# Kernel tuning notes

Hardware: AMD Instinct MI355X
Metric: run time of the kernel (lower is better)

The kernel has to match this reference:

```python
import jax, jax.numpy as jnp
import numpy as np

D_MODEL = 1024
N_HEAD = 16
HEAD_DIM = D_MODEL // N_HEAD


def setup_inputs() -> dict:
    key = jax.random.key(0)
    ks = jax.random.split(key, 5)
    B, T = 2, 2048
    s = 1.0 / np.sqrt(D_MODEL)
    return {
        "x": jax.random.normal(ks[0], (B, T, D_MODEL), dtype=jnp.float32),
        "w_qkv": jax.random.normal(ks[1], (D_MODEL, 3 * D_MODEL), dtype=jnp.float32) * s,
        "b_qkv": jnp.zeros((3 * D_MODEL,), dtype=jnp.float32),
        "w_proj": jax.random.normal(ks[2], (D_MODEL, D_MODEL), dtype=jnp.float32) * s,
        "b_proj": jnp.zeros((D_MODEL,), dtype=jnp.float32),
    }


def reference(x, w_qkv, b_qkv, w_proj, b_proj):
    B, T, C = x.shape
    H, Dh = N_HEAD, HEAD_DIM
    scale = Dh ** -0.5
    qkv = x @ w_qkv + b_qkv                      # [B,T,3C]
    q, k, v = jnp.split(qkv, 3, axis=2)
    # [B,T,C] -> [B,H,T,Dh]
    q = q.reshape(B, T, H, Dh).transpose(0, 2, 1, 3)
    k = k.reshape(B, T, H, Dh).transpose(0, 2, 1, 3)
    v = v.reshape(B, T, H, Dh).transpose(0, 2, 1, 3)
    att = jnp.einsum("bhqd,bhkd->bhqk", q, k) * scale  # [B,H,T,T]
    causal = jnp.tril(jnp.ones((T, T), dtype=bool))
    att = jnp.where(causal, att, -jnp.inf)
    att = jax.nn.softmax(att, axis=-1)
    out = jnp.einsum("bhqk,bhkd->bhqd", att, v)  # [B,H,T,Dh]
    out = out.transpose(0, 2, 1, 3).reshape(B, T, C)
    return out @ w_proj + b_proj
```

## Files before the change

kernel.cpp:

```cpp
#include <hip/hip_runtime.h>
#include <hip/hip_bf16.h>

#define B_ 2
#define T_ 2048
#define C_ 1024
#define H_ 16
#define DH_ 64

typedef __attribute__((ext_vector_type(8))) short bf16x8;
typedef __attribute__((ext_vector_type(4))) float f32x4;
typedef __attribute__((ext_vector_type(4))) unsigned int u32x4;

#define DEVI static __device__ __forceinline__

DEVI unsigned short f2bf(float f) {
  unsigned int u = __float_as_uint(f);
  u = (u + 0x7fffu + ((u >> 16) & 1u)) >> 16;
  return (unsigned short)u;
}

DEVI f32x4 mfma16(bf16x8 a, bf16x8 b, f32x4 c) {
  return __builtin_amdgcn_mfma_f32_16x16x32_bf16(a, b, c, 0, 0, 0);
}

DEVI void gload_lds16(const unsigned short* g, unsigned short* l) {
  __builtin_amdgcn_global_load_lds(
      (const __attribute__((address_space(1))) unsigned int*)g,
      (__attribute__((address_space(3))) unsigned int*)l, 16, 0, 0);
}

DEVI unsigned int cvtpk_bf16(float lo, float hi) {
  unsigned int r;
  asm("v_cvt_pk_bf16_f32 %0, %1, %2" : "=v"(r) : "v"(lo), "v"(hi));
  return r;
}

DEVI int kperm(int kv) {
  return (kv & 3) | (((kv >> 3) & 1) << 2) | (((kv >> 5) & 1) << 3) |
         (((kv >> 2) & 1) << 4) | (((kv >> 4) & 1) << 5);
}

__global__ __launch_bounds__(256) void prep_kernel(
    const float* __restrict__ x, const float* __restrict__ w_qkv,
    const float* __restrict__ w_proj, unsigned short* __restrict__ xb,
    unsigned short* __restrict__ wqkvT, unsigned short* __restrict__ wprojT) {
  __shared__ float tile[32][33];
  int b = blockIdx.x, tid = threadIdx.x;
  if (b < 4096) {
    int i = b * 256 + tid;
    float4 v = reinterpret_cast<const float4*>(x)[i];
    ushort4 o;
    o.x = f2bf(v.x); o.y = f2bf(v.y); o.z = f2bf(v.z); o.w = f2bf(v.w);
    reinterpret_cast<ushort4*>(xb)[i] = o;
  } else {
    const float* in;
    unsigned short* out;
    int R, C, bb;
    if (b < 7168) { bb = b - 4096; in = w_qkv; out = wqkvT; R = 1024; C = 3072; }
    else          { bb = b - 7168; in = w_proj; out = wprojT; R = 1024; C = 1024; }
    int nbx = C >> 5;
    int c0 = (bb % nbx) * 32, r0 = (bb / nbx) * 32;
    int tx = tid & 31, ty = tid >> 5;
#pragma unroll
    for (int j = 0; j < 32; j += 8)
      tile[ty + j][tx] = in[(size_t)(r0 + ty + j) * C + c0 + tx];
    __syncthreads();
#pragma unroll
    for (int j = 0; j < 32; j += 8)
      out[(size_t)(c0 + ty + j) * R + r0 + tx] = f2bf(tile[tx][ty + j]);
  }
}

__global__ __launch_bounds__(256, 2) void gemm192_qkv(
    const unsigned short* __restrict__ A, const unsigned short* __restrict__ Bt,
    const float* __restrict__ bias,
    unsigned short* __restrict__ qbuf, unsigned short* __restrict__ kbuf,
    unsigned short* __restrict__ vtbuf) {
  __shared__ __attribute__((aligned(16))) unsigned short As[2][128 * 64];
  __shared__ __attribute__((aligned(16))) unsigned short Bs[2][192 * 64];
  const int Kd = 1024;
  int tid = threadIdx.x;
  int lane = tid & 63, w = tid >> 6;
  int wn = w;
  int lrow = lane & 15, lgrp = lane >> 4;

  int g = blockIdx.x;
  int gs = (g & 7) * 64 + (g >> 3);
  int by = gs >> 4, bx = gs & 15;
  int bm = by * 128, bn = bx * 192;
  const unsigned short* Ab = A + (size_t)bm * Kd;
  const unsigned short* Bb = Bt + (size_t)bn * Kd;

  int sL[2], scl[2];
#pragma unroll
  for (int it = 0; it < 2; ++it) {
    int c = tid + it * 256;
    int L = c >> 3, s = c & 7, v = s ^ (L & 7);
    sL[it] = L;
    scl[it] = (v >> 2) * 32 + (v & 3) * 8;
  }

  auto stgA = [&](int t, int h) {
    unsigned short* dst = As[t & 1] + h * 4096;
    int k0 = t << 6;
#pragma unroll
    for (int it = 0; it < 2; ++it)
      gload_lds16(Ab + (size_t)(h * 64 + sL[it]) * Kd + k0 + scl[it],
                  dst + (tid + it * 256) * 8);
  };
  auto stgB3 = [&](int t, int th) {
    unsigned short* dst = Bs[t & 1] + th * 4096;
    int k0 = t << 6;
#pragma unroll
    for (int it = 0; it < 2; ++it)
      gload_lds16(Bb + (size_t)(th * 64 + sL[it]) * Kd + k0 + scl[it],
                  dst + (tid + it * 256) * 8);
  };

  auto lda = [&](const unsigned short* buf, int mi, int kk) -> bf16x8 {
    int row = mi * 16 + lrow;
    int s = ((kk << 2) | lgrp) ^ (row & 7);
    return *reinterpret_cast<const bf16x8*>((const char*)buf + row * 128 + s * 16);
  };
  auto ldb = [&](const unsigned short* buf, int ni, int kk) -> bf16x8 {
    int row = wn * 48 + ni * 16 + lrow;
    int s = ((kk << 2) | lgrp) ^ (row & 7);
    return *reinterpret_cast<const bf16x8*>((const char*)buf + row * 128 + s * 16);
  };

  f32x4 acc[8][3] = {};
  bf16x8 bfr[3][2], af[2][2];

#define PHASE_TAIL                                          \
  __builtin_amdgcn_s_barrier();                             \
  asm volatile("s_waitcnt lgkmcnt(0)" ::: "memory");        \
  __builtin_amdgcn_sched_barrier(0);                        \
  __builtin_amdgcn_s_setprio(1);

#define MFMA_TRI(base)                                      \
  _Pragma("unroll") for (int ii = 0; ii < 2; ++ii)          \
  _Pragma("unroll") for (int ni = 0; ni < 3; ++ni) {        \
    acc[(base) + ii][ni] = mfma16(af[ii][0], bfr[ni][0], acc[(base) + ii][ni]); \
    acc[(base) + ii][ni] = mfma16(af[ii][1], bfr[ni][1], acc[(base) + ii][ni]); \
  }

#define PHASE_END                                           \
  __builtin_amdgcn_s_setprio(0);                            \
  __builtin_amdgcn_s_barrier();

  stgA(0, 0); stgA(0, 1);
  stgB3(0, 0); stgB3(0, 1); stgB3(0, 2);
  stgB3(1, 0); stgB3(1, 1); stgB3(1, 2);
  asm volatile("s_waitcnt vmcnt(6)" ::: "memory");
  __builtin_amdgcn_s_barrier();

#pragma unroll 1
  for (int j = 0; j < 8; ++j) {
    const bool nl = (j < 7);
    const int t1 = 2 * j + 1, t2 = 2 * j + 2, t3 = 2 * j + 3;

#pragma unroll
    for (int ni = 0; ni < 3; ++ni) { bfr[ni][0] = ldb(Bs[0], ni, 0); bfr[ni][1] = ldb(Bs[0], ni, 1); }
    af[0][0] = lda(As[0], 0, 0); af[0][1] = lda(As[0], 0, 1);
    af[1][0] = lda(As[0], 1, 0); af[1][1] = lda(As[0], 1, 1);
    stgA(t1, 0);
    PHASE_TAIL; MFMA_TRI(0); PHASE_END;

    af[0][0] = lda(As[0], 2, 0); af[0][1] = lda(As[0], 2, 1);
    af[1][0] = lda(As[0], 3, 0); af[1][1] = lda(As[0], 3, 1);
    stgA(t1, 1);
    if (nl) stgB3(t2, 0);
    PHASE_TAIL; MFMA_TRI(2); PHASE_END;

    af[0][0] = lda(As[0], 4, 0); af[0][1] = lda(As[0], 4, 1);
    af[1][0] = lda(As[0], 5, 0); af[1][1] = lda(As[0], 5, 1);
    if (nl) stgB3(t2, 1);
    PHASE_TAIL; MFMA_TRI(4); PHASE_END;

    af[0][0] = lda(As[0], 6, 0); af[0][1] = lda(As[0], 6, 1);
    af[1][0] = lda(As[0], 7, 0); af[1][1] = lda(As[0], 7, 1);
    if (nl) stgB3(t2, 2);
    PHASE_TAIL; MFMA_TRI(6);
    __builtin_amdgcn_s_setprio(0);
    if (nl) { asm volatile("s_waitcnt vmcnt(6)" ::: "memory"); }
    else    { asm volatile("s_waitcnt vmcnt(0)" ::: "memory"); }
    __builtin_amdgcn_s_barrier();

#pragma unroll
    for (int ni = 0; ni < 3; ++ni) { bfr[ni][0] = ldb(Bs[1], ni, 0); bfr[ni][1] = ldb(Bs[1], ni, 1); }
    af[0][0] = lda(As[1], 0, 0); af[0][1] = lda(As[1], 0, 1);
    af[1][0] = lda(As[1], 1, 0); af[1][1] = lda(As[1], 1, 1);
    if (nl) stgA(t2, 0);
    PHASE_TAIL; MFMA_TRI(0); PHASE_END;

    af[0][0] = lda(As[1], 2, 0); af[0][1] = lda(As[1], 2, 1);
    af[1][0] = lda(As[1], 3, 0); af[1][1] = lda(As[1], 3, 1);
    if (nl) { stgA(t2, 1); stgB3(t3, 0); }
    PHASE_TAIL; MFMA_TRI(2); PHASE_END;

    af[0][0] = lda(As[1], 4, 0); af[0][1] = lda(As[1], 4, 1);
    af[1][0] = lda(As[1], 5, 0); af[1][1] = lda(As[1], 5, 1);
    if (nl) stgB3(t3, 1);
    PHASE_TAIL; MFMA_TRI(4); PHASE_END;

    af[0][0] = lda(As[1], 6, 0); af[0][1] = lda(As[1], 6, 1);
    af[1][0] = lda(As[1], 7, 0); af[1][1] = lda(As[1], 7, 1);
    if (nl) stgB3(t3, 2);
    PHASE_TAIL; MFMA_TRI(6);
    __builtin_amdgcn_s_setprio(0);
    if (nl) { asm volatile("s_waitcnt vmcnt(6)" ::: "memory"); }
    __builtin_amdgcn_s_barrier();
  }
#undef PHASE_TAIL
#undef MFMA_TRI
#undef PHASE_END

  int c0 = bn + wn * 48;
#pragma unroll
  for (int ni = 0; ni < 3; ++ni) {
    int col = c0 + ni * 16 + lrow;
    float bv = bias[col];
    int which = col >> 10, cc = col & 1023;
    int h = cc >> 6, d = cc & 63;
#pragma unroll
    for (int mi = 0; mi < 8; ++mi) {
      int rowb = bm + mi * 16 + lgrp * 4;
      int b = rowb >> 11, tt = rowb & 2047;
      if (which == 2) {
        ushort4 pk;
        pk.x = f2bf(acc[mi][ni][0] + bv);
        pk.y = f2bf(acc[mi][ni][1] + bv);
        pk.z = f2bf(acc[mi][ni][2] + bv);
        pk.w = f2bf(acc[mi][ni][3] + bv);
        *reinterpret_cast<ushort4*>(vtbuf + ((size_t)((b * 16 + h) * 64 + d)) * T_ + tt) = pk;
      } else {
        unsigned short* dst = (which == 0) ? qbuf : kbuf;
        size_t base = ((size_t)(b * 16 + h) * T_ + tt) * DH_ + d;
#pragma unroll
        for (int r = 0; r < 4; ++r)
          dst[base + (size_t)r * DH_] = f2bf(acc[mi][ni][r] + bv);
      }
    }
  }
}

__global__ __launch_bounds__(256, 2) void gemm_proj(
    const unsigned short* __restrict__ A, const unsigned short* __restrict__ Bt,
    const float* __restrict__ bias, float* __restrict__ outp) {
  __shared__ __attribute__((aligned(16))) unsigned short As[2][128 * 64];
  __shared__ __attribute__((aligned(16))) unsigned short Bs[2][128 * 64];
  const int Kd = 1024, Nd = 1024;
  int tid = threadIdx.x;
  int lane = tid & 63, w = tid >> 6;
  int wn = w;
  int lrow = lane & 15, lgrp = lane >> 4;

  int g = blockIdx.x;
  int gs = (g & 7) * 32 + (g >> 3);
  int by = gs >> 3, bx = gs & 7;
  int bm = by * 128, bn = bx * 128;
  const unsigned short* Ab = A + (size_t)bm * Kd;
  const unsigned short* Bb = Bt + (size_t)bn * Kd;

  int sL[2], scl[2];
#pragma unroll
  for (int it = 0; it < 2; ++it) {
    int c = tid + it * 256;
    int L = c >> 3, s = c & 7, v = s ^ (L & 7);
    sL[it] = L;
    scl[it] = (v >> 2) * 32 + (v & 3) * 8;
  }

  auto stgA = [&](int t, int h) {
    unsigned short* dst = As[t & 1] + h * 4096;
    int k0 = t << 6;
#pragma unroll
    for (int it = 0; it < 2; ++it)
      gload_lds16(Ab + (size_t)(h * 64 + sL[it]) * Kd + k0 + scl[it],
                  dst + (tid + it * 256) * 8);
  };
  auto stgB = [&](int t, int h) {
    unsigned short* dst = Bs[t & 1] + h * 4096;
    int k0 = t << 6;
#pragma unroll
    for (int it = 0; it < 2; ++it)
      gload_lds16(Bb + (size_t)(h * 64 + sL[it]) * Kd + k0 + scl[it],
                  dst + (tid + it * 256) * 8);
  };

  auto lda = [&](const unsigned short* buf, int mi, int kk) -> bf16x8 {
    int row = mi * 16 + lrow;
    int s = ((kk << 2) | lgrp) ^ (row & 7);
    return *reinterpret_cast<const bf16x8*>((const char*)buf + row * 128 + s * 16);
  };
  auto ldb = [&](const unsigned short* buf, int ni, int kk) -> bf16x8 {
    int row = wn * 32 + ni * 16 + lrow;
    int s = ((kk << 2) | lgrp) ^ (row & 7);
    return *reinterpret_cast<const bf16x8*>((const char*)buf + row * 128 + s * 16);
  };

  f32x4 acc[8][2] = {};
  bf16x8 bfr[2][2], af[2][2];

#define PHASE_TAIL                                          \
  __builtin_amdgcn_s_barrier();                             \
  asm volatile("s_waitcnt lgkmcnt(0)" ::: "memory");        \
  __builtin_amdgcn_sched_barrier(0);                        \
  __builtin_amdgcn_s_setprio(1);

#define MFMA_DUO(base)                                      \
  _Pragma("unroll") for (int ii = 0; ii < 2; ++ii)          \
  _Pragma("unroll") for (int ni = 0; ni < 2; ++ni) {        \
    acc[(base) + ii][ni] = mfma16(af[ii][0], bfr[ni][0], acc[(base) + ii][ni]); \
    acc[(base) + ii][ni] = mfma16(af[ii][1], bfr[ni][1], acc[(base) + ii][ni]); \
  }

#define PHASE_END                                           \
  __builtin_amdgcn_s_setprio(0);                            \
  __builtin_amdgcn_s_barrier();

  stgA(0, 0); stgA(0, 1); stgB(0, 0); stgB(0, 1);
  stgB(1, 0); stgB(1, 1);
  asm volatile("s_waitcnt vmcnt(4)" ::: "memory");
  __builtin_amdgcn_s_barrier();

#pragma unroll 1
  for (int j = 0; j < 8; ++j) {
    const bool nl = (j < 7);
    const int t1 = 2 * j + 1, t2 = 2 * j + 2, t3 = 2 * j + 3;

#pragma unroll
    for (int ni = 0; ni < 2; ++ni) { bfr[ni][0] = ldb(Bs[0], ni, 0); bfr[ni][1] = ldb(Bs[0], ni, 1); }
    af[0][0] = lda(As[0], 0, 0); af[0][1] = lda(As[0], 0, 1);
    af[1][0] = lda(As[0], 1, 0); af[1][1] = lda(As[0], 1, 1);
    stgA(t1, 0);
    PHASE_TAIL; MFMA_DUO(0); PHASE_END;

    af[0][0] = lda(As[0], 2, 0); af[0][1] = lda(As[0], 2, 1);
    af[1][0] = lda(As[0], 3, 0); af[1][1] = lda(As[0], 3, 1);
    stgA(t1, 1);
    if (nl) stgB(t2, 0);
    PHASE_TAIL; MFMA_DUO(2); PHASE_END;

    af[0][0] = lda(As[0], 4, 0); af[0][1] = lda(As[0], 4, 1);
    af[1][0] = lda(As[0], 5, 0); af[1][1] = lda(As[0], 5, 1);
    if (nl) stgB(t2, 1);
    PHASE_TAIL; MFMA_DUO(4); PHASE_END;

    af[0][0] = lda(As[0], 6, 0); af[0][1] = lda(As[0], 6, 1);
    af[1][0] = lda(As[0], 7, 0); af[1][1] = lda(As[0], 7, 1);
    PHASE_TAIL; MFMA_DUO(6);
    __builtin_amdgcn_s_setprio(0);
    if (nl) { asm volatile("s_waitcnt vmcnt(4)" ::: "memory"); }
    else    { asm volatile("s_waitcnt vmcnt(0)" ::: "memory"); }
    __builtin_amdgcn_s_barrier();

#pragma unroll
    for (int ni = 0; ni < 2; ++ni) { bfr[ni][0] = ldb(Bs[1], ni, 0); bfr[ni][1] = ldb(Bs[1], ni, 1); }
    af[0][0] = lda(As[1], 0, 0); af[0][1] = lda(As[1], 0, 1);
    af[1][0] = lda(As[1], 1, 0); af[1][1] = lda(As[1], 1, 1);
    if (nl) stgA(t2, 0);
    PHASE_TAIL; MFMA_DUO(0); PHASE_END;

    af[0][0] = lda(As[1], 2, 0); af[0][1] = lda(As[1], 2, 1);
    af[1][0] = lda(As[1], 3, 0); af[1][1] = lda(As[1], 3, 1);
    if (nl) { stgA(t2, 1); stgB(t3, 0); }
    PHASE_TAIL; MFMA_DUO(2); PHASE_END;

    af[0][0] = lda(As[1], 4, 0); af[0][1] = lda(As[1], 4, 1);
    af[1][0] = lda(As[1], 5, 0); af[1][1] = lda(As[1], 5, 1);
    if (nl) stgB(t3, 1);
    PHASE_TAIL; MFMA_DUO(4); PHASE_END;

    af[0][0] = lda(As[1], 6, 0); af[0][1] = lda(As[1], 6, 1);
    af[1][0] = lda(As[1], 7, 0); af[1][1] = lda(As[1], 7, 1);
    PHASE_TAIL; MFMA_DUO(6);
    __builtin_amdgcn_s_setprio(0);
    if (nl) { asm volatile("s_waitcnt vmcnt(4)" ::: "memory"); }
    __builtin_amdgcn_s_barrier();
  }
#undef PHASE_TAIL
#undef MFMA_DUO
#undef PHASE_END

  int c0 = bn + wn * 32;
#pragma unroll
  for (int ni = 0; ni < 2; ++ni) {
    int col = c0 + ni * 16 + lrow;
    float bv = bias[col];
#pragma unroll
    for (int mi = 0; mi < 8; ++mi) {
      int rowb = bm + mi * 16 + lgrp * 4;
#pragma unroll
      for (int r = 0; r < 4; ++r)
        outp[(size_t)(rowb + r) * Nd + col] = acc[mi][ni][r] + bv;
    }
  }
}

__global__ __launch_bounds__(256, 4) void attn_kernel(
    const unsigned short* __restrict__ qbuf,
    const unsigned short* __restrict__ kbuf,
    const unsigned short* __restrict__ vtbuf,
    unsigned short* __restrict__ attno) {
  __shared__ __attribute__((aligned(16))) unsigned short Ks[64 * 64];
  __shared__ __attribute__((aligned(16))) unsigned short Vts[64 * 64];

  int tid = threadIdx.x;
  int lane = tid & 63, w = tid >> 6;
  int lrow = lane & 15, lgrp = lane >> 4;

  int g = blockIdx.x;
  int s = g >> 8;
  int p = (g >> 3) & 7;
  int bh = (g & 7) | (((g >> 6) & 3) << 3);
  int qb = (s == 0) ? p : (s == 1) ? (31 - p) : (s == 2) ? (8 + p) : (23 - p);
  int wq0 = qb * 64 + w * 16;
  int nkb = qb + 1;

  const unsigned short* Qb = qbuf + (size_t)bh * T_ * DH_;
  const unsigned short* Kb = kbuf + (size_t)bh * T_ * DH_;
  const unsigned short* Vb = vtbuf + (size_t)bh * DH_ * T_;

  int srow0 = tid >> 3, scol = tid & 7;
  int srow1 = srow0 + 32;
  int pk0 = kperm(srow0), pk1 = kperm(srow1);
  int soffK0 = pk0 * 128 + ((scol * 16) ^ ((pk0 & 7) << 4));
  int soffK1 = pk1 * 128 + ((scol * 16) ^ ((pk1 & 7) << 4));
  int soffV0 = srow0 * 128 + ((scol * 16) ^ ((srow0 & 7) << 4));
  int soffV1 = srow1 * 128 + ((scol * 16) ^ ((srow1 & 7) << 4));

  const float SC = 0.125f * 1.44269504f;
  int kvbase = ((lgrp & 1) << 3) | ((lgrp >> 1) << 5);
  const int koff[4] = {0, 4, 16, 20};

  bf16x8 qf[2];
#pragma unroll
  for (int ks = 0; ks < 2; ++ks)
    qf[ks] = *reinterpret_cast<const bf16x8*>(
        Qb + (size_t)(wq0 + lrow) * DH_ + ks * 32 + lgrp * 8);

  f32x4 o[4] = {};
  float l_run = 0.f;

  bf16x8 sk0, sk1, sv0, sv1;
  auto stage_load = [&](int kb) {
    sk0 = *reinterpret_cast<const bf16x8*>(Kb + (size_t)(kb * 64 + srow0) * DH_ + scol * 8);
    sk1 = *reinterpret_cast<const bf16x8*>(Kb + (size_t)(kb * 64 + srow1) * DH_ + scol * 8);
    sv0 = *reinterpret_cast<const bf16x8*>(Vb + (size_t)srow0 * T_ + kb * 64 + scol * 8);
    sv1 = *reinterpret_cast<const bf16x8*>(Vb + (size_t)srow1 * T_ + kb * 64 + scol * 8);
  };
  auto stage_write = [&]() {
    *reinterpret_cast<bf16x8*>((char*)Ks + soffK0) = sk0;
    *reinterpret_cast<bf16x8*>((char*)Ks + soffK1) = sk1;
    *reinterpret_cast<bf16x8*>((char*)Vts + soffV0) = sv0;
    *reinterpret_cast<bf16x8*>((char*)Vts + soffV1) = sv1;
  };

  stage_load(0);
#pragma unroll 1
  for (int kb = 0; kb < nkb; ++kb) {
    if (kb > 0) __syncthreads();
    stage_write();
    __syncthreads();
    if (kb + 1 < nkb) stage_load(kb + 1);

    f32x4 sreg[4] = {};
#pragma unroll
    for (int ks = 0; ks < 2; ++ks) {
      bf16x8 kf[4];
#pragma unroll
      for (int ni = 0; ni < 4; ++ni) {
        int kr = ni * 16 + lrow;
        int off = kr * 128 + (((ks * 32 + lgrp * 8) * 2) ^ ((kr & 7) << 4));
        kf[ni] = *reinterpret_cast<const bf16x8*>((const char*)Ks + off);
      }
      __builtin_amdgcn_s_setprio(1);
#pragma unroll
      for (int ni = 0; ni < 4; ++ni)
        sreg[ni] = mfma16(kf[ni], qf[ks], sreg[ni]);
      __builtin_amdgcn_s_setprio(0);
    }

    if (kb == qb) {
      int q = wq0 + lrow;
#pragma unroll
      for (int ni = 0; ni < 4; ++ni) {
        int kvb = kb * 64 + kvbase + koff[ni];
#pragma unroll
        for (int r = 0; r < 4; ++r)
          if (kvb + r > q) sreg[ni][r] = -1e30f;
      }
    }

    f32x4 e[4];
#pragma unroll
    for (int ni = 0; ni < 4; ++ni)
#pragma unroll
      for (int r = 0; r < 4; ++r)
        e[ni][r] = __builtin_amdgcn_exp2f(sreg[ni][r] * SC);

    f32x4 ts = (e[0] + e[1]) + (e[2] + e[3]);
    l_run += (ts[0] + ts[1]) + (ts[2] + ts[3]);

    unsigned int Aw[4], Bw[4];
    Aw[0] = cvtpk_bf16(e[0][0], e[0][1]); Aw[1] = cvtpk_bf16(e[0][2], e[0][3]);
    Aw[2] = cvtpk_bf16(e[1][0], e[1][1]); Aw[3] = cvtpk_bf16(e[1][2], e[1][3]);
    Bw[0] = cvtpk_bf16(e[2][0], e[2][1]); Bw[1] = cvtpk_bf16(e[2][2], e[2][3]);
    Bw[2] = cvtpk_bf16(e[3][0], e[3][1]); Bw[3] = cvtpk_bf16(e[3][2], e[3][3]);
    u32x4 p0v, p1v;
#pragma unroll
    for (int ww = 0; ww < 4; ++ww) {
      auto sw = __builtin_amdgcn_permlane32_swap(Aw[ww], Bw[ww], false, false);
      p0v[ww] = sw[0];
      p1v[ww] = sw[1];
    }
    bf16x8 pa[2];
    pa[0] = __builtin_bit_cast(bf16x8, p0v);
    pa[1] = __builtin_bit_cast(bf16x8, p1v);

#pragma unroll
    for (int ks = 0; ks < 2; ++ks) {
      bf16x8 vf[4];
#pragma unroll
      for (int di = 0; di < 4; ++di) {
        int vr = di * 16 + lrow;
        int off = vr * 128 + (((ks * 32 + lgrp * 8) * 2) ^ ((vr & 7) << 4));
        vf[di] = *reinterpret_cast<const bf16x8*>((const char*)Vts + off);
      }
      __builtin_amdgcn_s_setprio(1);
#pragma unroll
      for (int di = 0; di < 4; ++di)
        o[di] = mfma16(pa[ks], vf[di], o[di]);
      __builtin_amdgcn_s_setprio(0);
    }
  }

  float rs = l_run;
  rs += __shfl_xor(rs, 16);
  rs += __shfl_xor(rs, 32);
  float linv = 1.0f / rs;

  int b = bh >> 4, h = bh & 15;
  float lr[4];
#pragma unroll
  for (int r = 0; r < 4; ++r) lr[r] = __shfl(linv, lgrp * 4 + r);
#pragma unroll
  for (int r = 0; r < 4; ++r) {
    int q = wq0 + lgrp * 4 + r;
    size_t base = ((size_t)(b * T_ + q)) * C_ + h * 64 + lrow;
#pragma unroll
    for (int di = 0; di < 4; ++di)
      attno[base + (size_t)di * 16] = f2bf(o[di][r] * lr[r]);
  }
}

extern "C" void kernel_launch(void* const* d_in, const int* in_sizes, int n_in,
                              void* d_out, int out_size, void* d_ws, size_t ws_size,
                              hipStream_t stream) {
  const float* x      = (const float*)d_in[0];
  const float* w_qkv  = (const float*)d_in[1];
  const float* b_qkv  = (const float*)d_in[2];
  const float* w_proj = (const float*)d_in[3];
  const float* b_proj = (const float*)d_in[4];

  char* ws = (char*)d_ws;
  unsigned short* xb     = (unsigned short*)(ws + 0);
  unsigned short* wqkvT  = (unsigned short*)(ws + 8388608);
  unsigned short* wprojT = (unsigned short*)(ws + 14680064);
  unsigned short* qbuf   = (unsigned short*)(ws + 16777216);
  unsigned short* kbuf   = (unsigned short*)(ws + 25165824);
  unsigned short* vtbuf  = (unsigned short*)(ws + 33554432);
  unsigned short* attno  = (unsigned short*)(ws + 41943040);

  prep_kernel<<<8192, 256, 0, stream>>>(x, w_qkv, w_proj, xb, wqkvT, wprojT);
  gemm192_qkv<<<dim3(512), 256, 0, stream>>>(xb, wqkvT, b_qkv, qbuf, kbuf, vtbuf);
  attn_kernel<<<dim3(1024), 256, 0, stream>>>(qbuf, kbuf, vtbuf, attno);
  gemm_proj<<<dim3(256), 256, 0, stream>>>(attno, wprojT, b_proj, (float*)d_out);
}
```

Baseline: 91.99 us.

## Split attention query tiles to 32 rows with 128-thread blocks

The attention kernel now uses 2048 blocks of 128 threads (two waves), each covering 32 query rows instead of 64, with a new tile ordering that interleaves short and long causal tiles. Each thread stages four K and four V vectors per key block to fill the shared tiles. The aim is finer-grained work for better load balance and occupancy under the causal triangle. In exchange, each K/V tile is loaded from global memory by twice as many blocks, and the diagonal block now masks the tile that holds the block's query rows.

```diff
diff --git a/kernel.cpp b/kernel.cpp
--- a/kernel.cpp
+++ b/kernel.cpp
@@ -398,7 +398,7 @@
   }
 }
 
-__global__ __launch_bounds__(256, 4) void attn_kernel(
+__global__ __launch_bounds__(128, 4) void attn_kernel(
     const unsigned short* __restrict__ qbuf,
     const unsigned short* __restrict__ kbuf,
     const unsigned short* __restrict__ vtbuf,
@@ -412,23 +412,27 @@
 
   int g = blockIdx.x;
   int s = g >> 8;
-  int p = (g >> 3) & 7;
-  int bh = (g & 7) | (((g >> 6) & 3) << 3);
-  int qb = (s == 0) ? p : (s == 1) ? (31 - p) : (s == 2) ? (8 + p) : (23 - p);
-  int wq0 = qb * 64 + w * 16;
-  int nkb = qb + 1;
+  int p = (g >> 5) & 7;
+  int bh = g & 31;
+  const int tbase[8] = {0, 63, 16, 47, 8, 55, 24, 39};
+  int qt = tbase[s] + ((s & 1) ? -p : p);
+  int wq0 = qt * 32 + w * 16;
+  int nkb = (qt >> 1) + 1;
 
   const unsigned short* Qb = qbuf + (size_t)bh * T_ * DH_;
   const unsigned short* Kb = kbuf + (size_t)bh * T_ * DH_;
   const unsigned short* Vb = vtbuf + (size_t)bh * DH_ * T_;
 
-  int srow0 = tid >> 3, scol = tid & 7;
-  int srow1 = srow0 + 32;
-  int pk0 = kperm(srow0), pk1 = kperm(srow1);
-  int soffK0 = pk0 * 128 + ((scol * 16) ^ ((pk0 & 7) << 4));
-  int soffK1 = pk1 * 128 + ((scol * 16) ^ ((pk1 & 7) << 4));
-  int soffV0 = srow0 * 128 + ((scol * 16) ^ ((srow0 & 7) << 4));
-  int soffV1 = srow1 * 128 + ((scol * 16) ^ ((srow1 & 7) << 4));
+  int srow = tid >> 1, sc4 = (tid & 1) * 4;
+  int Rk = kperm(srow);
+  int soffK[4], soffV[4], gcK[4];
+#pragma unroll
+  for (int j = 0; j < 4; ++j) {
+    int c = sc4 + j;
+    soffK[j] = Rk * 128 + ((c << 4) ^ ((Rk & 7) << 4));
+    soffV[j] = srow * 128 + ((c << 4) ^ ((srow & 7) << 4));
+    gcK[j] = c * 8;
+  }
 
   const float SC = 0.125f * 1.44269504f;
   int kvbase = ((lgrp & 1) << 3) | ((lgrp >> 1) << 5);
@@ -443,18 +447,20 @@
   f32x4 o[4] = {};
   float l_run = 0.f;
 
-  bf16x8 sk0, sk1, sv0, sv1;
+  bf16x8 skr[4], svr[4];
   auto stage_load = [&](int kb) {
-    sk0 = *reinterpret_cast<const bf16x8*>(Kb + (size_t)(kb * 64 + srow0) * DH_ + scol * 8);
-    sk1 = *reinterpret_cast<const bf16x8*>(Kb + (size_t)(kb * 64 + srow1) * DH_ + scol * 8);
-    sv0 = *reinterpret_cast<const bf16x8*>(Vb + (size_t)srow0 * T_ + kb * 64 + scol * 8);
-    sv1 = *reinterpret_cast<const bf16x8*>(Vb + (size_t)srow1 * T_ + kb * 64 + scol * 8);
+#pragma unroll
+    for (int j = 0; j < 4; ++j) {
+      skr[j] = *reinterpret_cast<const bf16x8*>(Kb + (size_t)(kb * 64 + srow) * DH_ + gcK[j]);
+      svr[j] = *reinterpret_cast<const bf16x8*>(Vb + (size_t)srow * T_ + kb * 64 + gcK[j]);
+    }
   };
   auto stage_write = [&]() {
-    *reinterpret_cast<bf16x8*>((char*)Ks + soffK0) = sk0;
-    *reinterpret_cast<bf16x8*>((char*)Ks + soffK1) = sk1;
-    *reinterpret_cast<bf16x8*>((char*)Vts + soffV0) = sv0;
-    *reinterpret_cast<bf16x8*>((char*)Vts + soffV1) = sv1;
+#pragma unroll
+    for (int j = 0; j < 4; ++j) {
+      *reinterpret_cast<bf16x8*>((char*)Ks + soffK[j]) = skr[j];
+      *reinterpret_cast<bf16x8*>((char*)Vts + soffV[j]) = svr[j];
+    }
   };
 
   stage_load(0);
@@ -482,7 +488,7 @@
       __builtin_amdgcn_s_setprio(0);
     }
 
-    if (kb == qb) {
+    if (kb == nkb - 1) {
       int q = wq0 + lrow;
 #pragma unroll
       for (int ni = 0; ni < 4; ++ni) {
@@ -575,6 +581,6 @@
 
   prep_kernel<<<8192, 256, 0, stream>>>(x, w_qkv, w_proj, xb, wqkvT, wprojT);
   gemm192_qkv<<<dim3(512), 256, 0, stream>>>(xb, wqkvT, b_qkv, qbuf, kbuf, vtbuf);
-  attn_kernel<<<dim3(1024), 256, 0, stream>>>(qbuf, kbuf, vtbuf, attno);
+  attn_kernel<<<dim3(2048), 128, 0, stream>>>(qbuf, kbuf, vtbuf, attno);
   gemm_proj<<<dim3(256), 256, 0, stream>>>(attno, wprojT, b_proj, (float*)d_out);
 }
```

Measured after the change: 105.0 us. +14.2%, slower.

## Split long causal query blocks across two KV halves and merge partial results

Applied to the files above, without the earlier changes.

The ten longest query blocks per head (qb 22–31) now each run as two workgroups. Each workgroup covers half of the key/value range and writes unnormalized fp32 partial outputs and row sums to workspace. A new merge kernel adds the two halves and normalizes into the bf16 attention output. The remaining blocks are issued longest-first, so the critical path drops from 32 key blocks to about 22. In exchange there is an extra kernel launch, more fp32 workspace traffic, and reuse of workspace regions that held already-consumed bf16 inputs.

```diff
diff --git a/kernel.cpp b/kernel.cpp
--- a/kernel.cpp
+++ b/kernel.cpp
@@ -402,7 +402,8 @@
     const unsigned short* __restrict__ qbuf,
     const unsigned short* __restrict__ kbuf,
     const unsigned short* __restrict__ vtbuf,
-    unsigned short* __restrict__ attno) {
+    unsigned short* __restrict__ attno,
+    float* __restrict__ opart, float* __restrict__ lpart) {
   __shared__ __attribute__((aligned(16))) unsigned short Ks[64 * 64];
   __shared__ __attribute__((aligned(16))) unsigned short Vts[64 * 64];
 
@@ -411,12 +412,13 @@
   int lrow = lane & 15, lgrp = lane >> 4;
 
   int g = blockIdx.x;
-  int s = g >> 8;
-  int p = (g >> 3) & 7;
-  int bh = (g & 7) | (((g >> 6) & 3) << 3);
-  int qb = (s == 0) ? p : (s == 1) ? (31 - p) : (s == 2) ? (8 + p) : (23 - p);
+  int bh = g & 31;
+  int s = g >> 5;
+  int qb, kb0, kbN, mode = 0, half = 0;
+  if (s < 22)      { qb = 21 - s;  kb0 = 0;              kbN = qb + 1;        }
+  else if (s < 32) { qb = s;       kb0 = 0;              kbN = (qb + 2) >> 1; mode = 1; half = 0; }
+  else             { qb = s - 10;  kb0 = (qb + 2) >> 1;  kbN = qb + 1;        mode = 1; half = 1; }
   int wq0 = qb * 64 + w * 16;
-  int nkb = qb + 1;
 
   const unsigned short* Qb = qbuf + (size_t)bh * T_ * DH_;
   const unsigned short* Kb = kbuf + (size_t)bh * T_ * DH_;
@@ -457,13 +459,13 @@
     *reinterpret_cast<bf16x8*>((char*)Vts + soffV1) = sv1;
   };
 
-  stage_load(0);
+  stage_load(kb0);
 #pragma unroll 1
-  for (int kb = 0; kb < nkb; ++kb) {
-    if (kb > 0) __syncthreads();
+  for (int kb = kb0; kb < kbN; ++kb) {
+    if (kb > kb0) __syncthreads();
     stage_write();
     __syncthreads();
-    if (kb + 1 < nkb) stage_load(kb + 1);
+    if (kb + 1 < kbN) stage_load(kb + 1);
 
     f32x4 sreg[4] = {};
 #pragma unroll
@@ -539,19 +541,56 @@
   float rs = l_run;
   rs += __shfl_xor(rs, 16);
   rs += __shfl_xor(rs, 32);
-  float linv = 1.0f / rs;
-
+
+  if (mode == 0) {
+    float linv = 1.0f / rs;
+    int b = bh >> 4, h = bh & 15;
+    float lr[4];
+#pragma unroll
+    for (int r = 0; r < 4; ++r) lr[r] = __shfl(linv, lgrp * 4 + r);
+#pragma unroll
+    for (int r = 0; r < 4; ++r) {
+      int q = wq0 + lgrp * 4 + r;
+      size_t base = ((size_t)(b * T_ + q)) * C_ + h * 64 + lrow;
+#pragma unroll
+      for (int di = 0; di < 4; ++di)
+        attno[base + (size_t)di * 16] = f2bf(o[di][r] * lr[r]);
+    }
+  } else {
+    int t = qb - 22;
+    float* ob = opart + ((size_t)((half * 32 + bh) * 10 + t)) * 4096;
+#pragma unroll
+    for (int r = 0; r < 4; ++r) {
+      int row = w * 16 + lgrp * 4 + r;
+#pragma unroll
+      for (int di = 0; di < 4; ++di)
+        ob[row * 64 + di * 16 + lrow] = o[di][r];
+    }
+    if (lgrp == 0)
+      lpart[((size_t)((half * 32 + bh) * 10 + t)) * 64 + w * 16 + lrow] = rs;
+  }
+}
+
+__global__ __launch_bounds__(256) void merge_kernel(
+    const float* __restrict__ opart, const float* __restrict__ lpart,
+    unsigned short* __restrict__ attno) {
+  int g = blockIdx.x;
+  int bh = g & 31, t = g >> 5;
+  int qb = 22 + t;
   int b = bh >> 4, h = bh & 15;
-  float lr[4];
-#pragma unroll
-  for (int r = 0; r < 4; ++r) lr[r] = __shfl(linv, lgrp * 4 + r);
-#pragma unroll
-  for (int r = 0; r < 4; ++r) {
-    int q = wq0 + lgrp * 4 + r;
-    size_t base = ((size_t)(b * T_ + q)) * C_ + h * 64 + lrow;
-#pragma unroll
-    for (int di = 0; di < 4; ++di)
-      attno[base + (size_t)di * 16] = f2bf(o[di][r] * lr[r]);
+  int tid = threadIdx.x;
+  int col = tid & 63, r0 = tid >> 6;
+  const float* o1 = opart + ((size_t)(bh * 10 + t)) * 4096;
+  const float* o2 = opart + ((size_t)((32 + bh) * 10 + t)) * 4096;
+  const float* l1 = lpart + ((size_t)(bh * 10 + t)) * 64;
+  const float* l2 = lpart + ((size_t)((32 + bh) * 10 + t)) * 64;
+#pragma unroll
+  for (int rr = 0; rr < 16; ++rr) {
+    int row = rr * 4 + r0;
+    float linv = 1.0f / (l1[row] + l2[row]);
+    float v = (o1[row * 64 + col] + o2[row * 64 + col]) * linv;
+    int q = qb * 64 + row;
+    attno[((size_t)(b * T_ + q)) * C_ + h * 64 + col] = f2bf(v);
   }
 }
 
@@ -572,9 +611,12 @@
   unsigned short* kbuf   = (unsigned short*)(ws + 25165824);
   unsigned short* vtbuf  = (unsigned short*)(ws + 33554432);
   unsigned short* attno  = (unsigned short*)(ws + 41943040);
+  float* opart = (float*)(ws + 0);
+  float* lpart = (float*)(ws + 11534336);
 
   prep_kernel<<<8192, 256, 0, stream>>>(x, w_qkv, w_proj, xb, wqkvT, wprojT);
   gemm192_qkv<<<dim3(512), 256, 0, stream>>>(xb, wqkvT, b_qkv, qbuf, kbuf, vtbuf);
-  attn_kernel<<<dim3(1024), 256, 0, stream>>>(qbuf, kbuf, vtbuf, attno);
+  attn_kernel<<<dim3(1344), 256, 0, stream>>>(qbuf, kbuf, vtbuf, attno, opart, lpart);
+  merge_kernel<<<dim3(320), 256, 0, stream>>>(opart, lpart, attno);
   gemm_proj<<<dim3(256), 256, 0, stream>>>(attno, wprojT, b_proj, (float*)d_out);
 }
```

After: 100.0 us. 1.09x slower.
